# Kernel tuning notes

Hardware: AMD Instinct MI355X
Metric: run time of the kernel (lower is better)

Reference implementation:

```python
import jax, jax.numpy as jnp
import numpy as np

HOPS = 3
VOCAB, EMBD, STORY_LEN, SENT_LEN, BATCH, QLEN = 50000, 128, 200, 32, 64, 32
INIT_RNG = 0.1


def setup_inputs() -> dict:
    key = jax.random.key(0)
    k1, k2, k3, k4, k5 = jax.random.split(key, 5)
    x = jax.random.randint(k1, (BATCH, STORY_LEN, SENT_LEN), 0, VOCAB)          # story token ids
    q = jax.random.randint(k2, (BATCH, QLEN), 0, VOCAB)                          # question token ids
    # hops+1 embedding tables, initialized ~ Normal(mean=-0.1, std=0.1) as in the torch code
    A = jax.random.normal(k3, (HOPS + 1, VOCAB, EMBD), dtype=jnp.float32) * INIT_RNG - INIT_RNG
    TA = jax.random.normal(k4, (STORY_LEN,), dtype=jnp.float32) * INIT_RNG - INIT_RNG
    TC = jax.random.normal(k5, (STORY_LEN,), dtype=jnp.float32) * INIT_RNG - INIT_RNG
    return {"A": A, "TA": TA, "TC": TC, "x": x, "q": q}


def reference(A, TA, TC, x, q):
    # dropout p=0.0 -> identity
    # u: question embedding, summed over query tokens -> [B, E]
    u = jnp.take(A[1], q, axis=0).sum(axis=1)
    for k in range(HOPS):
        # memory (m) and output (c) representations: gather + sum over sentence tokens + temporal encoding
        m = jnp.take(A[k], x, axis=0).sum(axis=2) + TA[None, :, None]      # [B, S, E]
        c = jnp.take(A[k + 1], x, axis=0).sum(axis=2) + TC[None, :, None]  # [B, S, E]
        p = jax.nn.softmax(jnp.einsum("bse,be->bs", m, u), axis=-1)        # attention over story [B, S]
        u = jnp.einsum("bse,bs->be", c, p) + u                              # weighted combine + residual
    logits = u @ A[HOPS].T                                                  # W = A[-1].weight.T -> [B, V]
    return jax.nn.log_softmax(logits, axis=-1)
```

## Files before the change

### kernel.cpp

```cpp
#include <hip/hip_runtime.h>
#include <math.h>

#define VOCAB 50000
#define EMBD  128
#define SLEN  200
#define TOK   32
#define BATCH 64
#define QLEN  32
#define NSENT (BATCH*SLEN)
#define TBL   ((size_t)VOCAB*EMBD)
#define NTILE 3125
#define GMAIN 25600

typedef short short8 __attribute__((ext_vector_type(8)));
typedef float f32x4  __attribute__((ext_vector_type(4)));
typedef unsigned u32x4 __attribute__((ext_vector_type(4)));

__device__ inline float bits2f(unsigned u){ union{unsigned u; float f;}c; c.u=u; return c.f; }
__device__ inline unsigned f2bits(float f){ union{float f; unsigned u;}c; c.f=f; return c.u; }
__device__ inline unsigned pack_bf16(float lo, float hi){
    unsigned ul = f2bits(lo), uh = f2bits(hi);
    unsigned rl = (ul + 0x7fffu + ((ul>>16)&1u)) >> 16;
    unsigned rh = (uh + 0x7fffu + ((uh>>16)&1u)) >> 16;
    return rl | (rh<<16);
}
__device__ inline unsigned short bf16of(float f){
    unsigned u = f2bits(f);
    return (unsigned short)((u + 0x7fffu + ((u>>16)&1u)) >> 16);
}

__device__ inline float waveSum(float v) {
    #pragma unroll
    for (int o = 32; o > 0; o >>= 1) v += __shfl_down(v, o, 64);
    return v;
}
__device__ inline float waveMax(float v) {
    #pragma unroll
    for (int o = 32; o > 0; o >>= 1) v = fmaxf(v, __shfl_down(v, o, 64));
    return v;
}

__global__ __launch_bounds__(256) void conv_kernel(
    const float* __restrict__ A, u32x4* __restrict__ Ab2)
{
    int o = blockIdx.x*256 + threadIdx.x;
    int v = o >> 6;
    int c = (o >> 3) & 7;
    int k = (o >> 1) & 3;
    int h = o & 1;
    const f32x4* src = (const f32x4*)(A + (size_t)k*TBL + (size_t)v*EMBD + c*16 + h*8);
    f32x4 a = src[0], b = src[1];
    u32x4 r;
    r.x = pack_bf16(a.x,a.y); r.y = pack_bf16(a.z,a.w);
    r.z = pack_bf16(b.x,b.y); r.w = pack_bf16(b.z,b.w);
    Ab2[o] = r;
}

__global__ __launch_bounds__(256) void gather_kernel(
    const unsigned* __restrict__ Ab2, const int* __restrict__ x,
    const int* __restrict__ q, float* __restrict__ G, float* __restrict__ uF)
{
    int B = blockIdx.x;
    int wid = threadIdx.x >> 6, lane = threadIdx.x & 63;
    if (B < GMAIN) {
        int c  = B & 7;
        int bs = (B >> 3)*4 + wid;
        int tok8 = lane >> 3, sub8 = lane & 7;
        int k = sub8 >> 1, half = sub8 & 1;
        const int* idxp = x + (size_t)bs * TOK;
        float a0=0.f,a1=0.f,a2=0.f,a3=0.f,a4=0.f,a5=0.f,a6=0.f,a7=0.f;
        #pragma unroll
        for (int r = 0; r < 4; r++) {
            int idx = idxp[r*8 + tok8];
            u32x4 v = *(const u32x4*)(Ab2 + (size_t)idx*256 + c*32 + k*8 + half*4);
            a0 += bits2f(v.x<<16); a1 += bits2f(v.x&0xffff0000u);
            a2 += bits2f(v.y<<16); a3 += bits2f(v.y&0xffff0000u);
            a4 += bits2f(v.z<<16); a5 += bits2f(v.z&0xffff0000u);
            a6 += bits2f(v.w<<16); a7 += bits2f(v.w&0xffff0000u);
        }
        #pragma unroll
        for (int o = 8; o <= 32; o <<= 1) {
            a0 += __shfl_xor(a0,o,64); a1 += __shfl_xor(a1,o,64);
            a2 += __shfl_xor(a2,o,64); a3 += __shfl_xor(a3,o,64);
            a4 += __shfl_xor(a4,o,64); a5 += __shfl_xor(a5,o,64);
            a6 += __shfl_xor(a6,o,64); a7 += __shfl_xor(a7,o,64);
        }
        if (tok8 < 2) {
            f32x4 rr;
            if (tok8 == 0) { rr.x=a0; rr.y=a1; rr.z=a2; rr.w=a3; }
            else           { rr.x=a4; rr.y=a5; rr.z=a6; rr.w=a7; }
            float* dst = G + ((size_t)k*NSENT + bs)*EMBD + c*16 + half*8 + tok8*4;
            *(f32x4*)dst = rr;
        }
    } else {
        int b = (B - GMAIN)*4 + wid;
        int tok8 = lane >> 3, c = lane & 7;
        const int* idxp = q + (size_t)b * QLEN;
        float ac[16];
        #pragma unroll
        for (int i = 0; i < 16; i++) ac[i] = 0.f;
        #pragma unroll
        for (int r = 0; r < 4; r++) {
            int idx = idxp[r*8 + tok8];
            const unsigned* base = Ab2 + (size_t)idx*256 + c*32 + 8;
            u32x4 v1 = *(const u32x4*)base;
            u32x4 v2 = *(const u32x4*)(base + 4);
            ac[0] += bits2f(v1.x<<16); ac[1] += bits2f(v1.x&0xffff0000u);
            ac[2] += bits2f(v1.y<<16); ac[3] += bits2f(v1.y&0xffff0000u);
            ac[4] += bits2f(v1.z<<16); ac[5] += bits2f(v1.z&0xffff0000u);
            ac[6] += bits2f(v1.w<<16); ac[7] += bits2f(v1.w&0xffff0000u);
            ac[8] += bits2f(v2.x<<16); ac[9] += bits2f(v2.x&0xffff0000u);
            ac[10]+= bits2f(v2.y<<16); ac[11]+= bits2f(v2.y&0xffff0000u);
            ac[12]+= bits2f(v2.z<<16); ac[13]+= bits2f(v2.z&0xffff0000u);
            ac[14]+= bits2f(v2.w<<16); ac[15]+= bits2f(v2.w&0xffff0000u);
        }
        #pragma unroll
        for (int o = 8; o <= 32; o <<= 1)
            #pragma unroll
            for (int i = 0; i < 16; i++) ac[i] += __shfl_xor(ac[i],o,64);
        if (tok8 < 4) {
            f32x4 rr;
            if      (tok8 == 0) { rr.x=ac[0];  rr.y=ac[1];  rr.z=ac[2];  rr.w=ac[3];  }
            else if (tok8 == 1) { rr.x=ac[4];  rr.y=ac[5];  rr.z=ac[6];  rr.w=ac[7];  }
            else if (tok8 == 2) { rr.x=ac[8];  rr.y=ac[9];  rr.z=ac[10]; rr.w=ac[11]; }
            else                { rr.x=ac[12]; rr.y=ac[13]; rr.z=ac[14]; rr.w=ac[15]; }
            *(f32x4*)(uF + (size_t)b*EMBD + c*16 + tok8*4) = rr;
        }
    }
}

__global__ __launch_bounds__(1024) void hops_kernel(
    const float* __restrict__ G, const float* __restrict__ uF,
    const float* __restrict__ TA, const float* __restrict__ TC,
    unsigned short* __restrict__ ub)
{
    int b = blockIdx.x;
    int t = threadIdx.x;
    int lane = t & 63, wid = t >> 6;
    __shared__ __align__(16) float Gs[SLEN*132];
    __shared__ __align__(16) float uL[EMBD];
    __shared__ float p[256];
    __shared__ float red[16], red2[16];
    __shared__ float pc[7*EMBD];

    if (t < EMBD) uL[t] = uF[(size_t)b * EMBD + t];
    __syncthreads();

    for (int k = 0; k < 3; k++) {
        float v = (t < EMBD) ? uL[t] : 0.f;
        v = waveSum(v);
        if (lane == 0) red[wid] = v;
        __syncthreads();
        float sumU = 0.f;
        #pragma unroll
        for (int i = 0; i < 16; i++) sumU += red[i];
        int s = t >> 2, qd = t & 3;
        if (s < SLEN) {
            const float4* u4 = (const float4*)uL;
            float dot = 0.f;
            if (k == 0) {
                const f32x4* g4 = (const f32x4*)(G + ((size_t)b*SLEN + s)*EMBD);
                #pragma unroll
                for (int e = 0; e < 8; e++) {
                    f32x4 gg = g4[qd*8+e];
                    float4 uu = u4[qd*8+e];
                    dot += gg.x*uu.x + gg.y*uu.y + gg.z*uu.z + gg.w*uu.w;
                }
            } else {
                const float4* g4 = (const float4*)(Gs + s*132);
                #pragma unroll
                for (int e = 0; e < 8; e++) {
                    float4 gg = g4[qd*8+e], uu = u4[qd*8+e];
                    dot += gg.x*uu.x + gg.y*uu.y + gg.z*uu.z + gg.w*uu.w;
                }
            }
            dot += __shfl_xor(dot, 1, 64);
            dot += __shfl_xor(dot, 2, 64);
            if (qd == 0) p[s] = dot + TA[s]*sumU;
        }
        __syncthreads();
        float mv = (t < SLEN) ? p[t] : -3.4e38f;
        mv = waveMax(mv);
        if (lane == 0) red[wid] = mv;
        __syncthreads();
        float M = -3.4e38f;
        #pragma unroll
        for (int i = 0; i < 16; i++) M = fmaxf(M, red[i]);
        __syncthreads();
        float ev = 0.f, tc = 0.f;
        if (t < SLEN) { ev = __expf(p[t] - M); p[t] = ev; tc = ev * TC[t]; }
        float sv = waveSum(ev);
        float tv = waveSum(tc);
        if (lane == 0) { red[wid] = sv; red2[wid] = tv; }
        __syncthreads();
        float sumP = 0.f, pTC = 0.f;
        #pragma unroll
        for (int i = 0; i < 16; i++) { sumP += red[i]; pTC += red2[i]; }
        const float* Gc = G + ((size_t)(k+1)*NSENT + (size_t)b*SLEN)*EMBD;
        int e = t & 127, ch = t >> 7;
        float acc = 0.f;
        for (int s2 = ch*25; s2 < ch*25 + 25; s2++) {
            float g = Gc[(size_t)s2*EMBD + e];
            Gs[s2*132 + e] = g;
            acc += p[s2] * g;
        }
        if (ch > 0) pc[(ch-1)*EMBD + e] = acc;
        __syncthreads();
        if (ch == 0) {
            #pragma unroll
            for (int c = 0; c < 7; c++) acc += pc[c*EMBD + e];
            uL[e] += (acc + pTC) / sumP;
        }
        __syncthreads();
    }
    if (t < EMBD) ub[(size_t)b * EMBD + t] = bf16of(uL[t]);
}

__global__ __launch_bounds__(256) void logits_mfma(
    const unsigned* __restrict__ Ab2, const unsigned short* __restrict__ ub,
    float* __restrict__ out, float* __restrict__ part)
{
    int w = blockIdx.x*4 + (threadIdx.x >> 6);
    if (w >= NTILE) return;
    int lane = threadIdx.x & 63;
    int col = lane & 15, quad = lane >> 4;
    int v0 = w * 16;

    short8 af[4][4];
    #pragma unroll
    for (int bt = 0; bt < 4; bt++)
        #pragma unroll
        for (int kc = 0; kc < 4; kc++)
            af[bt][kc] = *(const short8*)(ub + (bt*16 + col)*EMBD + kc*32 + quad*8);

    f32x4 acc[4];
    #pragma unroll
    for (int bt = 0; bt < 4; bt++) acc[bt] = (f32x4){0.f, 0.f, 0.f, 0.f};

    #pragma unroll
    for (int kc = 0; kc < 4; kc++) {
        int c = kc*2 + (quad>>1);
        const u32x4* bp = (const u32x4*)(Ab2 + (size_t)(v0+col)*256 + c*32 + 24 + (quad&1)*4);
        u32x4 braw = *bp;
        short8 bf = *(short8*)&braw;
        #pragma unroll
        for (int bt = 0; bt < 4; bt++)
            acc[bt] = __builtin_amdgcn_mfma_f32_16x16x32_bf16(af[bt][kc], bf, acc[bt], 0, 0, 0);
    }

    #pragma unroll
    for (int bt = 0; bt < 4; bt++) {
        #pragma unroll
        for (int r = 0; r < 4; r++) {
            int bI = bt*16 + quad*4 + r;
            out[(size_t)bI * VOCAB + v0 + col] = acc[bt][r];
        }
        #pragma unroll
        for (int r = 0; r < 4; r++) {
            float m = acc[bt][r];
            #pragma unroll
            for (int o = 1; o < 16; o <<= 1) m = fmaxf(m, __shfl_xor(m, o, 64));
            float se = __expf(acc[bt][r] - m);
            #pragma unroll
            for (int o = 1; o < 16; o <<= 1) se += __shfl_xor(se, o, 64);
            if (col == 0) {
                int bI = bt*16 + quad*4 + r;
                float2 pr; pr.x = m; pr.y = se;
                ((float2*)part)[(size_t)bI * NTILE + w] = pr;
            }
        }
    }
}

__global__ __launch_bounds__(256) void norm_kernel(
    float* __restrict__ out, const float* __restrict__ part)
{
    int b = blockIdx.x / 49, c = blockIdx.x % 49;
    int t = threadIdx.x, lane = t & 63, wid = t >> 6;
    __shared__ float sm[4], sl[4];
    const float2* P = (const float2*)part + (size_t)b * NTILE;
    float M = -3.4e38f, L = 0.f;
    for (int i = t; i < NTILE; i += 256) {
        float2 pr = P[i];
        float m2 = fmaxf(M, pr.x);
        L = L * __expf(M - m2) + pr.y * __expf(pr.x - m2);
        M = m2;
    }
    #pragma unroll
    for (int o = 1; o < 64; o <<= 1) {
        float Mo = __shfl_xor(M, o, 64), Lo = __shfl_xor(L, o, 64);
        float m2 = fmaxf(M, Mo);
        L = L * __expf(M - m2) + Lo * __expf(Mo - m2);
        M = m2;
    }
    if (lane == 0) { sm[wid] = M; sl[wid] = L; }
    __syncthreads();
    float Mf = -3.4e38f, Lf = 0.f;
    #pragma unroll
    for (int i = 0; i < 4; i++) {
        float m2 = fmaxf(Mf, sm[i]);
        Lf = Lf * __expf(Mf - m2) + sl[i] * __expf(sm[i] - m2);
        Mf = m2;
    }
    float lse = Mf + __logf(Lf);
    int f4 = c * 256 + t;
    if (f4 < VOCAB/4) {
        float4* rowp = (float4*)(out + (size_t)b * VOCAB);
        float4 v = rowp[f4];
        v.x -= lse; v.y -= lse; v.z -= lse; v.w -= lse;
        rowp[f4] = v;
    }
}

extern "C" void kernel_launch(void* const* d_in, const int* in_sizes, int n_in,
                              void* d_out, int out_size, void* d_ws, size_t ws_size,
                              hipStream_t stream)
{
    const float* A  = (const float*)d_in[0];
    const float* TA = (const float*)d_in[1];
    const float* TC = (const float*)d_in[2];
    const int*   x  = (const int*)d_in[3];
    const int*   q  = (const int*)d_in[4];
    float* out = (float*)d_out;

    unsigned* Ab2 = (unsigned*)d_ws;
    float* G   = (float*)((char*)d_ws + (size_t)4*TBL*2);
    float* uF  = G + (size_t)4*NSENT*EMBD;
    unsigned short* ubp = (unsigned short*)(uF + (size_t)BATCH*EMBD);
    float* part = (float*)(ubp + (size_t)BATCH*EMBD);

    conv_kernel  <<<VOCAB*64/256, 256, 0, stream>>>(A, (u32x4*)Ab2);
    gather_kernel<<<GMAIN + 16, 256, 0, stream>>>(Ab2, x, q, G, uF);
    hops_kernel  <<<BATCH, 1024, 0, stream>>>(G, uF, TA, TC, ubp);
    logits_mfma  <<<(NTILE+3)/4, 256, 0, stream>>>(Ab2, ubp, out, part);
    norm_kernel  <<<BATCH*49, 256, 0, stream>>>(out, part);
}
```

Before: 277.0 us.

## Store sentence sums in bf16, prefetch hop rows, fuse logits and normalization cooperatively

The gather kernel now writes the per-sentence embedding sums as bf16 instead of fp32, which halves the intermediate G traffic. The hops kernel issues its loads of the next C slice early into registers, so they overlap the softmax work. The logits and norm kernels are merged into one cooperative kernel: it keeps logits in registers across a grid sync, reduces the log-sum-exp per row, and writes the output once, avoiding a read-modify-write pass over the 64x50000 output. The trade-offs are extra bf16 rounding in the memory sums, a grid fixed at 256 blocks that must be co-resident, and two grid-wide barriers.

```diff
diff --git a/kernel.cpp b/kernel.cpp
--- a/kernel.cpp
+++ b/kernel.cpp
@@ -1,5 +1,8 @@
 #include <hip/hip_runtime.h>
+#include <hip/hip_cooperative_groups.h>
 #include <math.h>
+
+namespace cg = cooperative_groups;
 
 #define VOCAB 50000
 #define EMBD  128
@@ -11,6 +14,7 @@
 #define TBL   ((size_t)VOCAB*EMBD)
 #define NTILE 3125
 #define GMAIN 25600
+#define NWAVE 1024
 
 typedef short short8 __attribute__((ext_vector_type(8)));
 typedef float f32x4  __attribute__((ext_vector_type(4)));
@@ -58,7 +62,8 @@
 
 __global__ __launch_bounds__(256) void gather_kernel(
     const unsigned* __restrict__ Ab2, const int* __restrict__ x,
-    const int* __restrict__ q, float* __restrict__ G, float* __restrict__ uF)
+    const int* __restrict__ q, unsigned short* __restrict__ Gb,
+    float* __restrict__ uF)
 {
     int B = blockIdx.x;
     int wid = threadIdx.x >> 6, lane = threadIdx.x & 63;
@@ -85,12 +90,11 @@
             a4 += __shfl_xor(a4,o,64); a5 += __shfl_xor(a5,o,64);
             a6 += __shfl_xor(a6,o,64); a7 += __shfl_xor(a7,o,64);
         }
-        if (tok8 < 2) {
-            f32x4 rr;
-            if (tok8 == 0) { rr.x=a0; rr.y=a1; rr.z=a2; rr.w=a3; }
-            else           { rr.x=a4; rr.y=a5; rr.z=a6; rr.w=a7; }
-            float* dst = G + ((size_t)k*NSENT + bs)*EMBD + c*16 + half*8 + tok8*4;
-            *(f32x4*)dst = rr;
+        if (tok8 == 0) {
+            u32x4 w;
+            w.x = pack_bf16(a0,a1); w.y = pack_bf16(a2,a3);
+            w.z = pack_bf16(a4,a5); w.w = pack_bf16(a6,a7);
+            *(u32x4*)(Gb + ((size_t)k*NSENT + bs)*EMBD + c*16 + half*8) = w;
         }
     } else {
         int b = (B - GMAIN)*4 + wid;
@@ -130,7 +134,7 @@
 }
 
 __global__ __launch_bounds__(1024) void hops_kernel(
-    const float* __restrict__ G, const float* __restrict__ uF,
+    const unsigned short* __restrict__ Gb, const float* __restrict__ uF,
     const float* __restrict__ TA, const float* __restrict__ TC,
     unsigned short* __restrict__ ub)
 {
@@ -146,7 +150,12 @@
     if (t < EMBD) uL[t] = uF[(size_t)b * EMBD + t];
     __syncthreads();
 
+    int e = t & 127, ch = t >> 7;
     for (int k = 0; k < 3; k++) {
+        const unsigned short* Gc = Gb + ((size_t)(k+1)*NSENT + (size_t)b*SLEN)*EMBD;
+        unsigned short pre[25];
+        #pragma unroll
+        for (int j = 0; j < 25; j++) pre[j] = Gc[(size_t)(ch*25+j)*EMBD + e];
         float v = (t < EMBD) ? uL[t] : 0.f;
         v = waveSum(v);
         if (lane == 0) red[wid] = v;
@@ -159,18 +168,22 @@
             const float4* u4 = (const float4*)uL;
             float dot = 0.f;
             if (k == 0) {
-                const f32x4* g4 = (const f32x4*)(G + ((size_t)b*SLEN + s)*EMBD);
-                #pragma unroll
-                for (int e = 0; e < 8; e++) {
-                    f32x4 gg = g4[qd*8+e];
-                    float4 uu = u4[qd*8+e];
-                    dot += gg.x*uu.x + gg.y*uu.y + gg.z*uu.z + gg.w*uu.w;
+                const u32x4* gb = (const u32x4*)(Gb + ((size_t)b*SLEN + s)*EMBD);
+                #pragma unroll
+                for (int i = 0; i < 4; i++) {
+                    u32x4 gv = gb[qd*4 + i];
+                    float4 u0 = u4[qd*8 + i*2];
+                    float4 u1 = u4[qd*8 + i*2 + 1];
+                    dot += bits2f(gv.x<<16)*u0.x + bits2f(gv.x&0xffff0000u)*u0.y
+                         + bits2f(gv.y<<16)*u0.z + bits2f(gv.y&0xffff0000u)*u0.w
+                         + bits2f(gv.z<<16)*u1.x + bits2f(gv.z&0xffff0000u)*u1.y
+                         + bits2f(gv.w<<16)*u1.z + bits2f(gv.w&0xffff0000u)*u1.w;
                 }
             } else {
                 const float4* g4 = (const float4*)(Gs + s*132);
                 #pragma unroll
-                for (int e = 0; e < 8; e++) {
-                    float4 gg = g4[qd*8+e], uu = u4[qd*8+e];
+                for (int i = 0; i < 8; i++) {
+                    float4 gg = g4[qd*8+i], uu = u4[qd*8+i];
                     dot += gg.x*uu.x + gg.y*uu.y + gg.z*uu.z + gg.w*uu.w;
                 }
             }
@@ -196,13 +209,12 @@
         float sumP = 0.f, pTC = 0.f;
         #pragma unroll
         for (int i = 0; i < 16; i++) { sumP += red[i]; pTC += red2[i]; }
-        const float* Gc = G + ((size_t)(k+1)*NSENT + (size_t)b*SLEN)*EMBD;
-        int e = t & 127, ch = t >> 7;
         float acc = 0.f;
-        for (int s2 = ch*25; s2 < ch*25 + 25; s2++) {
-            float g = Gc[(size_t)s2*EMBD + e];
-            Gs[s2*132 + e] = g;
-            acc += p[s2] * g;
+        #pragma unroll
+        for (int j = 0; j < 25; j++) {
+            float g = bits2f((unsigned)pre[j] << 16);
+            Gs[(ch*25+j)*132 + e] = g;
+            acc += p[ch*25+j] * g;
         }
         if (ch > 0) pc[(ch-1)*EMBD + e] = acc;
         __syncthreads();
@@ -216,15 +228,15 @@
     if (t < EMBD) ub[(size_t)b * EMBD + t] = bf16of(uL[t]);
 }
 
-__global__ __launch_bounds__(256) void logits_mfma(
+__global__ __launch_bounds__(256) void logits_coop(
     const unsigned* __restrict__ Ab2, const unsigned short* __restrict__ ub,
-    float* __restrict__ out, float* __restrict__ part)
-{
-    int w = blockIdx.x*4 + (threadIdx.x >> 6);
-    if (w >= NTILE) return;
+    float* __restrict__ out, float2* __restrict__ part, float* __restrict__ lse)
+{
+    cg::grid_group grid = cg::this_grid();
+    __shared__ float sm[4], sl[4];
+    int waveId = blockIdx.x*4 + (threadIdx.x >> 6);
     int lane = threadIdx.x & 63;
     int col = lane & 15, quad = lane >> 4;
-    int v0 = w * 16;
 
     short8 af[4][4];
     #pragma unroll
@@ -233,82 +245,103 @@
         for (int kc = 0; kc < 4; kc++)
             af[bt][kc] = *(const short8*)(ub + (bt*16 + col)*EMBD + kc*32 + quad*8);
 
-    f32x4 acc[4];
-    #pragma unroll
-    for (int bt = 0; bt < 4; bt++) acc[bt] = (f32x4){0.f, 0.f, 0.f, 0.f};
-
-    #pragma unroll
-    for (int kc = 0; kc < 4; kc++) {
-        int c = kc*2 + (quad>>1);
-        const u32x4* bp = (const u32x4*)(Ab2 + (size_t)(v0+col)*256 + c*32 + 24 + (quad&1)*4);
-        u32x4 braw = *bp;
-        short8 bf = *(short8*)&braw;
+    f32x4 acc[4][4];
+    float Mr[16], Lr[16];
+    #pragma unroll
+    for (int i = 0; i < 16; i++) { Mr[i] = -3.4e38f; Lr[i] = 0.f; }
+
+    #pragma unroll
+    for (int sl2 = 0; sl2 < 4; sl2++) {
+        int w = waveId + sl2*NWAVE;
+        if (w < NTILE) {
+            int v0 = w*16;
+            #pragma unroll
+            for (int bt = 0; bt < 4; bt++) acc[sl2][bt] = (f32x4){0.f,0.f,0.f,0.f};
+            #pragma unroll
+            for (int kc = 0; kc < 4; kc++) {
+                int c = kc*2 + (quad>>1);
+                u32x4 braw = *(const u32x4*)(Ab2 + (size_t)(v0+col)*256 + c*32 + 24 + (quad&1)*4);
+                short8 bf = *(short8*)&braw;
+                #pragma unroll
+                for (int bt = 0; bt < 4; bt++)
+                    acc[sl2][bt] = __builtin_amdgcn_mfma_f32_16x16x32_bf16(af[bt][kc], bf, acc[sl2][bt], 0, 0, 0);
+            }
+            #pragma unroll
+            for (int bt = 0; bt < 4; bt++)
+                #pragma unroll
+                for (int r = 0; r < 4; r++) {
+                    float m = acc[sl2][bt][r];
+                    #pragma unroll
+                    for (int o = 1; o < 16; o <<= 1) m = fmaxf(m, __shfl_xor(m, o, 64));
+                    float se = __expf(acc[sl2][bt][r] - m);
+                    #pragma unroll
+                    for (int o = 1; o < 16; o <<= 1) se += __shfl_xor(se, o, 64);
+                    int i = bt*4 + r;
+                    float nm = fmaxf(Mr[i], m);
+                    Lr[i] = Lr[i]*__expf(Mr[i]-nm) + se*__expf(m-nm);
+                    Mr[i] = nm;
+                }
+        }
+    }
+    if (col == 0) {
         #pragma unroll
         for (int bt = 0; bt < 4; bt++)
-            acc[bt] = __builtin_amdgcn_mfma_f32_16x16x32_bf16(af[bt][kc], bf, acc[bt], 0, 0, 0);
-    }
-
-    #pragma unroll
-    for (int bt = 0; bt < 4; bt++) {
-        #pragma unroll
-        for (int r = 0; r < 4; r++) {
-            int bI = bt*16 + quad*4 + r;
-            out[(size_t)bI * VOCAB + v0 + col] = acc[bt][r];
-        }
-        #pragma unroll
-        for (int r = 0; r < 4; r++) {
-            float m = acc[bt][r];
-            #pragma unroll
-            for (int o = 1; o < 16; o <<= 1) m = fmaxf(m, __shfl_xor(m, o, 64));
-            float se = __expf(acc[bt][r] - m);
-            #pragma unroll
-            for (int o = 1; o < 16; o <<= 1) se += __shfl_xor(se, o, 64);
-            if (col == 0) {
-                int bI = bt*16 + quad*4 + r;
-                float2 pr; pr.x = m; pr.y = se;
-                ((float2*)part)[(size_t)bI * NTILE + w] = pr;
+            #pragma unroll
+            for (int r = 0; r < 4; r++) {
+                int row = bt*16 + quad*4 + r;
+                float2 pr; pr.x = Mr[bt*4+r]; pr.y = Lr[bt*4+r];
+                part[(size_t)row*NWAVE + waveId] = pr;
             }
-        }
-    }
-}
-
-__global__ __launch_bounds__(256) void norm_kernel(
-    float* __restrict__ out, const float* __restrict__ part)
-{
-    int b = blockIdx.x / 49, c = blockIdx.x % 49;
-    int t = threadIdx.x, lane = t & 63, wid = t >> 6;
-    __shared__ float sm[4], sl[4];
-    const float2* P = (const float2*)part + (size_t)b * NTILE;
-    float M = -3.4e38f, L = 0.f;
-    for (int i = t; i < NTILE; i += 256) {
-        float2 pr = P[i];
-        float m2 = fmaxf(M, pr.x);
-        L = L * __expf(M - m2) + pr.y * __expf(pr.x - m2);
-        M = m2;
-    }
-    #pragma unroll
-    for (int o = 1; o < 64; o <<= 1) {
-        float Mo = __shfl_xor(M, o, 64), Lo = __shfl_xor(L, o, 64);
-        float m2 = fmaxf(M, Mo);
-        L = L * __expf(M - m2) + Lo * __expf(Mo - m2);
-        M = m2;
-    }
-    if (lane == 0) { sm[wid] = M; sl[wid] = L; }
-    __syncthreads();
-    float Mf = -3.4e38f, Lf = 0.f;
-    #pragma unroll
-    for (int i = 0; i < 4; i++) {
-        float m2 = fmaxf(Mf, sm[i]);
-        Lf = Lf * __expf(Mf - m2) + sl[i] * __expf(sm[i] - m2);
-        Mf = m2;
-    }
-    float lse = Mf + __logf(Lf);
-    int f4 = c * 256 + t;
-    if (f4 < VOCAB/4) {
-        float4* rowp = (float4*)(out + (size_t)b * VOCAB);
-        float4 v = rowp[f4];
-        v.x -= lse; v.y -= lse; v.z -= lse; v.w -= lse;
-        rowp[f4] = v;
+    }
+    __threadfence();
+    grid.sync();
+
+    if (blockIdx.x < BATCH) {
+        int row = blockIdx.x;
+        float M = -3.4e38f, L = 0.f;
+        for (int i = threadIdx.x; i < NWAVE; i += 256) {
+            float2 pr = part[(size_t)row*NWAVE + i];
+            float nm = fmaxf(M, pr.x);
+            L = L*__expf(M-nm) + pr.y*__expf(pr.x-nm);
+            M = nm;
+        }
+        #pragma unroll
+        for (int o = 1; o < 64; o <<= 1) {
+            float Mo = __shfl_xor(M,o,64), Lo = __shfl_xor(L,o,64);
+            float nm = fmaxf(M,Mo);
+            L = L*__expf(M-nm) + Lo*__expf(Mo-nm);
+            M = nm;
+        }
+        int wid = threadIdx.x >> 6;
+        if ((threadIdx.x & 63) == 0) { sm[wid] = M; sl[wid] = L; }
+        __syncthreads();
+        if (threadIdx.x == 0) {
+            float Mf = -3.4e38f, Lf = 0.f;
+            #pragma unroll
+            for (int i2 = 0; i2 < 4; i2++) {
+                float nm = fmaxf(Mf, sm[i2]);
+                Lf = Lf*__expf(Mf-nm) + sl[i2]*__expf(sm[i2]-nm);
+                Mf = nm;
+            }
+            lse[row] = Mf + __logf(Lf);
+        }
+    }
+    __threadfence();
+    grid.sync();
+
+    #pragma unroll
+    for (int sl2 = 0; sl2 < 4; sl2++) {
+        int w = waveId + sl2*NWAVE;
+        if (w < NTILE) {
+            int v0 = w*16;
+            #pragma unroll
+            for (int bt = 0; bt < 4; bt++)
+                #pragma unroll
+                for (int r = 0; r < 4; r++) {
+                    int row = bt*16 + quad*4 + r;
+                    out[(size_t)row*VOCAB + v0 + col] = acc[sl2][bt][r] - lse[row];
+                }
+        }
     }
 }
 
@@ -324,14 +357,24 @@
     float* out = (float*)d_out;
 
     unsigned* Ab2 = (unsigned*)d_ws;
-    float* G   = (float*)((char*)d_ws + (size_t)4*TBL*2);
-    float* uF  = G + (size_t)4*NSENT*EMBD;
+    unsigned short* Gb = (unsigned short*)((char*)d_ws + (size_t)4*TBL*2);
+    float* uF = (float*)(Gb + (size_t)4*NSENT*EMBD);
     unsigned short* ubp = (unsigned short*)(uF + (size_t)BATCH*EMBD);
-    float* part = (float*)(ubp + (size_t)BATCH*EMBD);
+    float2* part = (float2*)(ubp + (size_t)BATCH*EMBD);
+    float* lseP = (float*)(part + (size_t)BATCH*NWAVE);
 
     conv_kernel  <<<VOCAB*64/256, 256, 0, stream>>>(A, (u32x4*)Ab2);
-    gather_kernel<<<GMAIN + 16, 256, 0, stream>>>(Ab2, x, q, G, uF);
-    hops_kernel  <<<BATCH, 1024, 0, stream>>>(G, uF, TA, TC, ubp);
-    logits_mfma  <<<(NTILE+3)/4, 256, 0, stream>>>(Ab2, ubp, out, part);
-    norm_kernel  <<<BATCH*49, 256, 0, stream>>>(out, part);
-}
+    gather_kernel<<<GMAIN + 16, 256, 0, stream>>>(Ab2, x, q, Gb, uF);
+    hops_kernel  <<<BATCH, 1024, 0, stream>>>(Gb, uF, TA, TC, ubp);
+
+    void* args[5];
+    const unsigned* pAb2 = Ab2;
+    const unsigned short* pub = ubp;
+    args[0] = (void*)&pAb2;
+    args[1] = (void*)&pub;
+    args[2] = (void*)&out;
+    args[3] = (void*)&part;
+    args[4] = (void*)&lseP;
+    hipLaunchCooperativeKernel((const void*)logits_coop, dim3(256), dim3(256),
+                               args, 0, stream);
+}
```

New measurement: 383.3 us. 38.4% more time.

## Store gathered sentence sums as bf16 and prefetch hop memory before reductions

Applied to the files above, without the earlier changes.

The gather kernel now packs the summed sentence embeddings into bf16 instead of fp32, halving the intermediate G buffer traffic written by gather and read by the hops kernel. The hops kernel unpacks bf16 for the first-hop dot product. It also issues the loads for the next C memory slice into registers at the top of each hop, so their latency overlaps the attention reductions. This adds an extra rounding of the sums and more register pressure in a 1024-thread block.

```diff
diff --git a/kernel.cpp b/kernel.cpp
--- a/kernel.cpp
+++ b/kernel.cpp
@@ -58,7 +58,8 @@
 
 __global__ __launch_bounds__(256) void gather_kernel(
     const unsigned* __restrict__ Ab2, const int* __restrict__ x,
-    const int* __restrict__ q, float* __restrict__ G, float* __restrict__ uF)
+    const int* __restrict__ q, unsigned short* __restrict__ Gb,
+    float* __restrict__ uF)
 {
     int B = blockIdx.x;
     int wid = threadIdx.x >> 6, lane = threadIdx.x & 63;
@@ -85,12 +86,11 @@
             a4 += __shfl_xor(a4,o,64); a5 += __shfl_xor(a5,o,64);
             a6 += __shfl_xor(a6,o,64); a7 += __shfl_xor(a7,o,64);
         }
-        if (tok8 < 2) {
-            f32x4 rr;
-            if (tok8 == 0) { rr.x=a0; rr.y=a1; rr.z=a2; rr.w=a3; }
-            else           { rr.x=a4; rr.y=a5; rr.z=a6; rr.w=a7; }
-            float* dst = G + ((size_t)k*NSENT + bs)*EMBD + c*16 + half*8 + tok8*4;
-            *(f32x4*)dst = rr;
+        if (tok8 == 0) {
+            u32x4 w;
+            w.x = pack_bf16(a0,a1); w.y = pack_bf16(a2,a3);
+            w.z = pack_bf16(a4,a5); w.w = pack_bf16(a6,a7);
+            *(u32x4*)(Gb + ((size_t)k*NSENT + bs)*EMBD + c*16 + half*8) = w;
         }
     } else {
         int b = (B - GMAIN)*4 + wid;
@@ -130,7 +130,7 @@
 }
 
 __global__ __launch_bounds__(1024) void hops_kernel(
-    const float* __restrict__ G, const float* __restrict__ uF,
+    const unsigned short* __restrict__ Gb, const float* __restrict__ uF,
     const float* __restrict__ TA, const float* __restrict__ TC,
     unsigned short* __restrict__ ub)
 {
@@ -146,7 +146,12 @@
     if (t < EMBD) uL[t] = uF[(size_t)b * EMBD + t];
     __syncthreads();
 
+    int e = t & 127, ch = t >> 7;
     for (int k = 0; k < 3; k++) {
+        const unsigned short* Gc = Gb + ((size_t)(k+1)*NSENT + (size_t)b*SLEN)*EMBD;
+        unsigned short pre[25];
+        #pragma unroll
+        for (int j = 0; j < 25; j++) pre[j] = Gc[(size_t)(ch*25+j)*EMBD + e];
         float v = (t < EMBD) ? uL[t] : 0.f;
         v = waveSum(v);
         if (lane == 0) red[wid] = v;
@@ -159,18 +164,22 @@
             const float4* u4 = (const float4*)uL;
             float dot = 0.f;
             if (k == 0) {
-                const f32x4* g4 = (const f32x4*)(G + ((size_t)b*SLEN + s)*EMBD);
+                const u32x4* gb = (const u32x4*)(Gb + ((size_t)b*SLEN + s)*EMBD);
                 #pragma unroll
-                for (int e = 0; e < 8; e++) {
-                    f32x4 gg = g4[qd*8+e];
-                    float4 uu = u4[qd*8+e];
-                    dot += gg.x*uu.x + gg.y*uu.y + gg.z*uu.z + gg.w*uu.w;
+                for (int i = 0; i < 4; i++) {
+                    u32x4 gv = gb[qd*4 + i];
+                    float4 u0 = u4[qd*8 + i*2];
+                    float4 u1 = u4[qd*8 + i*2 + 1];
+                    dot += bits2f(gv.x<<16)*u0.x + bits2f(gv.x&0xffff0000u)*u0.y
+                         + bits2f(gv.y<<16)*u0.z + bits2f(gv.y&0xffff0000u)*u0.w
+                         + bits2f(gv.z<<16)*u1.x + bits2f(gv.z&0xffff0000u)*u1.y
+                         + bits2f(gv.w<<16)*u1.z + bits2f(gv.w&0xffff0000u)*u1.w;
                 }
             } else {
                 const float4* g4 = (const float4*)(Gs + s*132);
                 #pragma unroll
-                for (int e = 0; e < 8; e++) {
-                    float4 gg = g4[qd*8+e], uu = u4[qd*8+e];
+                for (int i = 0; i < 8; i++) {
+                    float4 gg = g4[qd*8+i], uu = u4[qd*8+i];
                     dot += gg.x*uu.x + gg.y*uu.y + gg.z*uu.z + gg.w*uu.w;
                 }
             }
@@ -196,13 +205,12 @@
         float sumP = 0.f, pTC = 0.f;
         #pragma unroll
         for (int i = 0; i < 16; i++) { sumP += red[i]; pTC += red2[i]; }
-        const float* Gc = G + ((size_t)(k+1)*NSENT + (size_t)b*SLEN)*EMBD;
-        int e = t & 127, ch = t >> 7;
         float acc = 0.f;
-        for (int s2 = ch*25; s2 < ch*25 + 25; s2++) {
-            float g = Gc[(size_t)s2*EMBD + e];
-            Gs[s2*132 + e] = g;
-            acc += p[s2] * g;
+        #pragma unroll
+        for (int j = 0; j < 25; j++) {
+            float g = bits2f((unsigned)pre[j] << 16);
+            Gs[(ch*25+j)*132 + e] = g;
+            acc += p[ch*25+j] * g;
         }
         if (ch > 0) pc[(ch-1)*EMBD + e] = acc;
         __syncthreads();
@@ -324,14 +332,14 @@
     float* out = (float*)d_out;
 
     unsigned* Ab2 = (unsigned*)d_ws;
-    float* G   = (float*)((char*)d_ws + (size_t)4*TBL*2);
-    float* uF  = G + (size_t)4*NSENT*EMBD;
+    unsigned short* Gb = (unsigned short*)((char*)d_ws + (size_t)4*TBL*2);
+    float* uF = (float*)(Gb + (size_t)4*NSENT*EMBD);
     unsigned short* ubp = (unsigned short*)(uF + (size_t)BATCH*EMBD);
     float* part = (float*)(ubp + (size_t)BATCH*EMBD);
 
     conv_kernel  <<<VOCAB*64/256, 256, 0, stream>>>(A, (u32x4*)Ab2);
-    gather_kernel<<<GMAIN + 16, 256, 0, stream>>>(Ab2, x, q, G, uF);
-    hops_kernel  <<<BATCH, 1024, 0, stream>>>(G, uF, TA, TC, ubp);
+    gather_kernel<<<GMAIN + 16, 256, 0, stream>>>(Ab2, x, q, Gb, uF);
+    hops_kernel  <<<BATCH, 1024, 0, stream>>>(Gb, uF, TA, TC, ubp);
     logits_mfma  <<<(NTILE+3)/4, 256, 0, stream>>>(Ab2, ubp, out, part);
     norm_kernel  <<<BATCH*49, 256, 0, stream>>>(out, part);
 }
```

After: 275.0 us. No clear change (-0.7%).
